# Optimization experiments

Measured on AMD Instinct MI355X. Metric: run time of the kernel, lower is better.

## Reference

```python
import jax, jax.numpy as jnp
import numpy as np

NP = 44
B = 400000

def setup_inputs() -> dict:
    key = jax.random.key(0)
    ks = jax.random.split(key, 9)
    return {
        "X":    jax.random.normal(ks[0], (NP, 1, B), dtype=jnp.float32),
        "lin1": jax.random.normal(ks[1], (NP, 4, 1), dtype=jnp.float32),
        "lin2": jax.random.normal(ks[2], (NP, 8, 4), dtype=jnp.float32),
        "lin3": jax.random.normal(ks[3], (NP, 4, 8), dtype=jnp.float32),
        "lin4": jax.random.normal(ks[4], (NP, 1, 4), dtype=jnp.float32),
        "b1":   jax.random.normal(ks[5], (NP, 4, 1), dtype=jnp.float32),
        "b2":   jax.random.normal(ks[6], (NP, 8, 1), dtype=jnp.float32),
        "b3":   jax.random.normal(ks[7], (NP, 4, 1), dtype=jnp.float32),
        "b4":   jax.random.normal(ks[8], (NP, 1, 1), dtype=jnp.float32),
    }

def reference(X, lin1, lin2, lin3, lin4, b1, b2, b3, b4):
    # forward_all: three relu(W @ X + b) layers, then a final affine layer.
    # Batched over NP populations ('l'), broadcast over the huge sample dim ('j').
    h = jax.nn.relu(jnp.einsum('lik,lkj->lij', lin1, X) + b1)   # (NP, 4, B)
    h = jax.nn.relu(jnp.einsum('lik,lkj->lij', lin2, h) + b2)   # (NP, 8, B)
    h = jax.nn.relu(jnp.einsum('lik,lkj->lij', lin3, h) + b3)   # (NP, 4, B)
    out = jnp.einsum('lik,lkj->lij', lin4, h) + b4              # (NP, 1, B)
    return out
```

## Files before the change

kernel.cpp:

```cpp
#include <hip/hip_runtime.h>


#define NP 44
#define BATCH 400000

typedef float v2f __attribute__((ext_vector_type(2)));
typedef float v4f __attribute__((ext_vector_type(4)));

__device__ __forceinline__ v2f splat(float s) { return (v2f){s, s}; }

__device__ __forceinline__ v2f mlp_pair(v2f x,
                                        const float* __restrict__ w1,
                                        const float* __restrict__ w2,
                                        const float* __restrict__ w3,
                                        const float* __restrict__ w4,
                                        const float* __restrict__ c1,
                                        const float* __restrict__ c2,
                                        const float* __restrict__ c3,
                                        float c4) {
    const v2f zero = splat(0.0f);
    v2f h1[4], h2[8], h3[4];
#pragma unroll
    for (int i = 0; i < 4; ++i) {
        v2f a = __builtin_elementwise_fma(splat(w1[i]), x, splat(c1[i]));
        h1[i] = __builtin_elementwise_max(a, zero);
    }
#pragma unroll
    for (int i = 0; i < 8; ++i) {
        v2f a = splat(c2[i]);
#pragma unroll
        for (int k = 0; k < 4; ++k)
            a = __builtin_elementwise_fma(splat(w2[i * 4 + k]), h1[k], a);
        h2[i] = __builtin_elementwise_max(a, zero);
    }
#pragma unroll
    for (int i = 0; i < 4; ++i) {
        v2f a = splat(c3[i]);
#pragma unroll
        for (int k = 0; k < 8; ++k)
            a = __builtin_elementwise_fma(splat(w3[i * 8 + k]), h2[k], a);
        h3[i] = __builtin_elementwise_max(a, zero);
    }
    v2f o = splat(c4);
#pragma unroll
    for (int k = 0; k < 4; ++k)
        o = __builtin_elementwise_fma(splat(w4[k]), h3[k], o);
    return o;
}

__global__ __launch_bounds__(256) void mlp_fwd_kernel(
        const float* __restrict__ X,
        const float* __restrict__ lin1,
        const float* __restrict__ lin2,
        const float* __restrict__ lin3,
        const float* __restrict__ lin4,
        const float* __restrict__ b1,
        const float* __restrict__ b2,
        const float* __restrict__ b3,
        const float* __restrict__ b4,
        float* __restrict__ out) {
    const int l = blockIdx.y;
    const int j4 = blockIdx.x * blockDim.x + threadIdx.x;
    constexpr int B4 = BATCH / 4;

    float w1[4], w4[4], c1[4], c3[4], w2[32], w3[32], c2[8];
#pragma unroll
    for (int i = 0; i < 4; ++i) {
        w1[i] = lin1[l * 4 + i];
        w4[i] = lin4[l * 4 + i];
        c1[i] = b1[l * 4 + i];
        c3[i] = b3[l * 4 + i];
    }
#pragma unroll
    for (int i = 0; i < 32; ++i) {
        w2[i] = lin2[l * 32 + i];
        w3[i] = lin3[l * 32 + i];
    }
#pragma unroll
    for (int i = 0; i < 8; ++i)
        c2[i] = b2[l * 8 + i];
    const float c4 = b4[l];

    if (j4 >= B4) return;

    const v4f* __restrict__ xin = (const v4f*)(X + (size_t)l * BATCH);
    v4f* po = (v4f*)(out + (size_t)l * BATCH);

    v4f x = xin[j4];
    v2f p0 = mlp_pair((v2f){x.x, x.y}, w1, w2, w3, w4, c1, c2, c3, c4);
    v2f p1 = mlp_pair((v2f){x.z, x.w}, w1, w2, w3, w4, c1, c2, c3, c4);

    v4f r = (v4f){p0.x, p0.y, p1.x, p1.y};
    __builtin_nontemporal_store(r, po + j4);
}

extern "C" void kernel_launch(void* const* d_in, const int* in_sizes, int n_in,
                              void* d_out, int out_size, void* d_ws, size_t ws_size,
                              hipStream_t stream) {
    const float* X    = (const float*)d_in[0];
    const float* lin1 = (const float*)d_in[1];
    const float* lin2 = (const float*)d_in[2];
    const float* lin3 = (const float*)d_in[3];
    const float* lin4 = (const float*)d_in[4];
    const float* b1   = (const float*)d_in[5];
    const float* b2   = (const float*)d_in[6];
    const float* b3   = (const float*)d_in[7];
    const float* b4   = (const float*)d_in[8];
    float* out = (float*)d_out;

    constexpr int B4 = BATCH / 4;
    dim3 block(256);
    dim3 grid((B4 + 255) / 256, NP);
    mlp_fwd_kernel<<<grid, block, 0, stream>>>(X, lin1, lin2, lin3, lin4,
                                               b1, b2, b3, b4, out);
}
```

Baseline: 140.7 us.

## Compute hidden MLP layers in packed fp16 with grid-stride loop

Converts inputs, weights and biases to packed half2 and runs the three hidden layers with packed fp16 FMA/max, keeping only the final affine layer in fp32. This targets the ALU-bound inner MLP by doubling elements per packed instruction. The grid becomes a fixed 49 blocks per population with a grid-stride loop, amortizing the per-thread weight loads across iterations. It risks precision loss and overflow from fp16 intermediates versus the fp32 reference.

```diff
diff --git a/kernel.cpp b/kernel.cpp
--- a/kernel.cpp
+++ b/kernel.cpp
@@ -3,49 +3,57 @@
 
 #define NP 44
 #define BATCH 400000
+#define B4C (BATCH / 4)
+#define GRIDX 49
 
 typedef float v2f __attribute__((ext_vector_type(2)));
 typedef float v4f __attribute__((ext_vector_type(4)));
+typedef _Float16 h2 __attribute__((ext_vector_type(2)));
 
-__device__ __forceinline__ v2f splat(float s) { return (v2f){s, s}; }
+__device__ __forceinline__ h2 hsplat(float s) {
+    _Float16 h = (_Float16)s;
+    return (h2){h, h};
+}
 
-__device__ __forceinline__ v2f mlp_pair(v2f x,
-                                        const float* __restrict__ w1,
-                                        const float* __restrict__ w2,
-                                        const float* __restrict__ w3,
-                                        const float* __restrict__ w4,
-                                        const float* __restrict__ c1,
-                                        const float* __restrict__ c2,
-                                        const float* __restrict__ c3,
-                                        float c4) {
-    const v2f zero = splat(0.0f);
-    v2f h1[4], h2[8], h3[4];
+__device__ __forceinline__ h2 pk_cvt(float a, float b) {
+    return __builtin_bit_cast(h2, __builtin_amdgcn_cvt_pkrtz(a, b));
+}
+
+__device__ __forceinline__ v2f mlp_pair(h2 x,
+        const h2* __restrict__ w1, const h2* __restrict__ w2,
+        const h2* __restrict__ w3, const h2* __restrict__ c1,
+        const h2* __restrict__ c2, const h2* __restrict__ c3,
+        const float* __restrict__ w4, float c4) {
+    const h2 zero = (h2){(_Float16)0.0f, (_Float16)0.0f};
+    h2 h1[4], t2[8], h3[4];
 #pragma unroll
     for (int i = 0; i < 4; ++i) {
-        v2f a = __builtin_elementwise_fma(splat(w1[i]), x, splat(c1[i]));
+        h2 a = __builtin_elementwise_fma(w1[i], x, c1[i]);
         h1[i] = __builtin_elementwise_max(a, zero);
     }
 #pragma unroll
     for (int i = 0; i < 8; ++i) {
-        v2f a = splat(c2[i]);
+        h2 a = c2[i];
 #pragma unroll
         for (int k = 0; k < 4; ++k)
-            a = __builtin_elementwise_fma(splat(w2[i * 4 + k]), h1[k], a);
-        h2[i] = __builtin_elementwise_max(a, zero);
+            a = __builtin_elementwise_fma(w2[i * 4 + k], h1[k], a);
+        t2[i] = __builtin_elementwise_max(a, zero);
     }
 #pragma unroll
     for (int i = 0; i < 4; ++i) {
-        v2f a = splat(c3[i]);
+        h2 a = c3[i];
 #pragma unroll
         for (int k = 0; k < 8; ++k)
-            a = __builtin_elementwise_fma(splat(w3[i * 8 + k]), h2[k], a);
+            a = __builtin_elementwise_fma(w3[i * 8 + k], t2[k], a);
         h3[i] = __builtin_elementwise_max(a, zero);
     }
-    v2f o = splat(c4);
+    float o0 = c4, o1 = c4;
 #pragma unroll
-    for (int k = 0; k < 4; ++k)
-        o = __builtin_elementwise_fma(splat(w4[k]), h3[k], o);
-    return o;
+    for (int k = 0; k < 4; ++k) {
+        o0 = fmaf(w4[k], (float)h3[k].x, o0);
+        o1 = fmaf(w4[k], (float)h3[k].y, o1);
+    }
+    return (v2f){o0, o1};
 }
 
 __global__ __launch_bounds__(256) void mlp_fwd_kernel(
@@ -60,38 +68,39 @@
         const float* __restrict__ b4,
         float* __restrict__ out) {
     const int l = blockIdx.y;
-    const int j4 = blockIdx.x * blockDim.x + threadIdx.x;
-    constexpr int B4 = BATCH / 4;
 
-    float w1[4], w4[4], c1[4], c3[4], w2[32], w3[32], c2[8];
+    h2 w1[4], c1[4], w2[32], c2[8], w3[32], c3[4];
+    float w4[4];
 #pragma unroll
     for (int i = 0; i < 4; ++i) {
-        w1[i] = lin1[l * 4 + i];
+        w1[i] = hsplat(lin1[l * 4 + i]);
+        c1[i] = hsplat(b1[l * 4 + i]);
+        c3[i] = hsplat(b3[l * 4 + i]);
         w4[i] = lin4[l * 4 + i];
-        c1[i] = b1[l * 4 + i];
-        c3[i] = b3[l * 4 + i];
     }
 #pragma unroll
     for (int i = 0; i < 32; ++i) {
-        w2[i] = lin2[l * 32 + i];
-        w3[i] = lin3[l * 32 + i];
+        w2[i] = hsplat(lin2[l * 32 + i]);
+        w3[i] = hsplat(lin3[l * 32 + i]);
     }
 #pragma unroll
     for (int i = 0; i < 8; ++i)
-        c2[i] = b2[l * 8 + i];
+        c2[i] = hsplat(b2[l * 8 + i]);
     const float c4 = b4[l];
-
-    if (j4 >= B4) return;
 
     const v4f* __restrict__ xin = (const v4f*)(X + (size_t)l * BATCH);
     v4f* po = (v4f*)(out + (size_t)l * BATCH);
 
-    v4f x = xin[j4];
-    v2f p0 = mlp_pair((v2f){x.x, x.y}, w1, w2, w3, w4, c1, c2, c3, c4);
-    v2f p1 = mlp_pair((v2f){x.z, x.w}, w1, w2, w3, w4, c1, c2, c3, c4);
-
-    v4f r = (v4f){p0.x, p0.y, p1.x, p1.y};
-    __builtin_nontemporal_store(r, po + j4);
+    for (int j4 = blockIdx.x * blockDim.x + threadIdx.x; j4 < B4C;
+         j4 += GRIDX * 256) {
+        v4f x = xin[j4];
+        h2 xa = pk_cvt(x.x, x.y);
+        h2 xb = pk_cvt(x.z, x.w);
+        v2f p0 = mlp_pair(xa, w1, w2, w3, c1, c2, c3, w4, c4);
+        v2f p1 = mlp_pair(xb, w1, w2, w3, c1, c2, c3, w4, c4);
+        v4f r = (v4f){p0.x, p0.y, p1.x, p1.y};
+        __builtin_nontemporal_store(r, po + j4);
+    }
 }
 
 extern "C" void kernel_launch(void* const* d_in, const int* in_sizes, int n_in,
@@ -108,9 +117,8 @@
     const float* b4   = (const float*)d_in[8];
     float* out = (float*)d_out;
 
-    constexpr int B4 = BATCH / 4;
     dim3 block(256);
-    dim3 grid((B4 + 255) / 256, NP);
+    dim3 grid(GRIDX, NP);
     mlp_fwd_kernel<<<grid, block, 0, stream>>>(X, lin1, lin2, lin3, lin4,
                                                b1, b2, b3, b4, out);
 }
```

Measured after the change: 144.2 us. 1.02x slower.
